# Performance work log

Measured on AMD Instinct MI355X. Metric: run time of the kernel, lower is better.

The kernel has to match this reference:

```python
import jax, jax.numpy as jnp
import numpy as np

B, C, H, W = 8, 256, 128, 128  # dim=256 channels, match_factor=2 -> num_matching=128


def setup_inputs() -> dict:
    key = jax.random.key(0)
    k1, k2 = jax.random.split(key)
    x = jax.random.normal(k1, (B, C, H, W), dtype=jnp.float32)
    Ym = jax.random.normal(k2, (B, C, H, W), dtype=jnp.float32)
    return {"x": x, "Ym": Ym, "num_matching": 128}


def _matching(x, Ym, num_matching):
    # x, Ym: (B, C, H, W); flatten spatial -> (B, C, N) with N = H*W
    b, c, h, w = x.shape
    xf = x.reshape(b, c, h * w)
    yf = Ym.reshape(b, c, h * w)
    # pairwise L2 distances between channel vectors: (B, C, C)
    x2 = jnp.sum(xf * xf, axis=-1)
    y2 = jnp.sum(yf * yf, axis=-1)
    d2 = x2[:, :, None] + y2[:, None, :] - 2.0 * jnp.einsum('bin,bjn->bij', xf, yf)
    dist = jnp.sqrt(jnp.maximum(d2, 0.0))
    # topk(k=1, largest=False) == min / argmin over candidates
    topk_values = jnp.min(dist, axis=-1)      # (B, C)
    topk_indices = jnp.argmin(dist, axis=-1)  # (B, C) nearest candidate per input channel
    # keep the num_matching input channels with smallest min-distance, in original order
    order = jnp.argsort(topk_values, axis=1)[:, :num_matching]  # channel ids with rank < num_matching
    sel = jnp.sort(order, axis=1)                               # restore original channel order (masked_select semantics)
    nn_idx = jnp.take_along_axis(topk_indices, sel, axis=1)     # (B, num_matching)
    # batched gather of candidate rows: (B, num_matching, N)
    filt = jnp.take_along_axis(yf, nn_idx[:, :, None], axis=1)
    return filt.reshape(b, num_matching, h, w)


def reference(x, Ym, num_matching):
    return _matching(x, Ym, num_matching)
```

## Files before the change

### kernel.cpp

```cpp
#include <hip/hip_runtime.h>

#define B_  8
#define C_  256
#define N_  16384
#define NM_ 128
#define LDK 40

typedef _Float16 f16x8 __attribute__((ext_vector_type(8)));
typedef float    f32x4 __attribute__((ext_vector_type(4)));

__global__ __launch_bounds__(512)
__attribute__((amdgpu_waves_per_eu(4, 4)))
void gemm_f16_kernel(const float* __restrict__ X,
                     const float* __restrict__ Y,
                     float* __restrict__ Gp,
                     float* __restrict__ x2p,
                     float* __restrict__ y2p,
                     int Kchunk) {
    __shared__ _Float16 aH[2][128][LDK];
    __shared__ _Float16 aL[2][128][LDK];
    __shared__ _Float16 bH[2][128][LDK];
    __shared__ _Float16 bL[2][128][LDK];

    int lin = blockIdx.x;
    int jt = lin & 1, it = (lin >> 1) & 1, b = (lin >> 2) & 7, ks = lin >> 5;
    int k0 = ks * Kchunk;

    int t = threadIdx.x;
    int lane = t & 63;
    int wid = t >> 6;
    int wm = wid >> 1, wn = wid & 1;

    int srow = t >> 2;
    int skq = (t & 3) * 8;

    const float* xp = X + ((size_t)(b * C_) + it * 128 + srow) * N_ + k0 + skq;
    const float* yp = Y + ((size_t)(b * C_) + jt * 128 + srow) * N_ + k0 + skq;

    f32x4 acc[2][4] = {};
    float sx = 0.f, sy = 0.f;
    float4 VA[2], VB[2];

    auto prefetch = [&](int koff) {
        VA[0] = *(const float4*)(xp + koff);
        VA[1] = *(const float4*)(xp + koff + 4);
        VB[0] = *(const float4*)(yp + koff);
        VB[1] = *(const float4*)(yp + koff + 4);
    };

    auto stage_chunk = [&](int bi) {
        _Float16 ha[8], la[8], hb[8], lb[8];
        const float* fa = (const float*)VA;
        const float* fb = (const float*)VB;
#pragma unroll
        for (int e = 0; e < 8; ++e) {
            float v = fa[e];
            _Float16 h = (_Float16)v;
            ha[e] = h; la[e] = (_Float16)(v - (float)h);
            sx += v * v;
            float w = fb[e];
            _Float16 h2 = (_Float16)w;
            hb[e] = h2; lb[e] = (_Float16)(w - (float)h2);
            sy += w * w;
        }
        *(f16x8*)&aH[bi][srow][skq] = *(f16x8*)&ha[0];
        *(f16x8*)&aL[bi][srow][skq] = *(f16x8*)&la[0];
        *(f16x8*)&bH[bi][srow][skq] = *(f16x8*)&hb[0];
        *(f16x8*)&bL[bi][srow][skq] = *(f16x8*)&lb[0];
    };

    prefetch(0);
    stage_chunk(0);
    if (Kchunk > 32) prefetch(32);

    int fr = lane & 15, fk = (lane >> 4) * 8;
    int cur = 0;

    for (int kk = 0; kk < Kchunk; kk += 32) {
        __syncthreads();

        f16x8 fAH0 = *(const f16x8*)&aH[cur][wm * 32 +  0 + fr][fk];
        f16x8 fAH1 = *(const f16x8*)&aH[cur][wm * 32 + 16 + fr][fk];
        f16x8 fAL0 = *(const f16x8*)&aL[cur][wm * 32 +  0 + fr][fk];
        f16x8 fAL1 = *(const f16x8*)&aL[cur][wm * 32 + 16 + fr][fk];

        if (kk + 32 < Kchunk) stage_chunk(cur ^ 1);
        if (kk + 64 < Kchunk) prefetch(kk + 64);

#pragma unroll
        for (int nf = 0; nf < 4; ++nf) {
            f16x8 fBH = *(const f16x8*)&bH[cur][wn * 64 + nf * 16 + fr][fk];
            f16x8 fBL = *(const f16x8*)&bL[cur][wn * 64 + nf * 16 + fr][fk];
            acc[0][nf] = __builtin_amdgcn_mfma_f32_16x16x32_f16(fAH0, fBH, acc[0][nf], 0, 0, 0);
            acc[1][nf] = __builtin_amdgcn_mfma_f32_16x16x32_f16(fAH1, fBH, acc[1][nf], 0, 0, 0);
            acc[0][nf] = __builtin_amdgcn_mfma_f32_16x16x32_f16(fAH0, fBL, acc[0][nf], 0, 0, 0);
            acc[1][nf] = __builtin_amdgcn_mfma_f32_16x16x32_f16(fAH1, fBL, acc[1][nf], 0, 0, 0);
            acc[0][nf] = __builtin_amdgcn_mfma_f32_16x16x32_f16(fAL0, fBH, acc[0][nf], 0, 0, 0);
            acc[1][nf] = __builtin_amdgcn_mfma_f32_16x16x32_f16(fAL1, fBH, acc[1][nf], 0, 0, 0);
        }
        cur ^= 1;
    }

    size_t gb = ((size_t)(ks * B_ + b) * C_ + it * 128) * C_ + jt * 128;
#pragma unroll
    for (int mf = 0; mf < 2; ++mf)
#pragma unroll
        for (int nf = 0; nf < 4; ++nf) {
            int rr = wm * 32 + mf * 16 + (lane >> 4) * 4;
            int cc = wn * 64 + nf * 16 + (lane & 15);
#pragma unroll
            for (int r = 0; r < 4; ++r)
                Gp[gb + (size_t)(rr + r) * C_ + cc] = acc[mf][nf][r];
        }

    sx += __shfl_xor(sx, 1);
    sx += __shfl_xor(sx, 2);
    sy += __shfl_xor(sy, 1);
    sy += __shfl_xor(sy, 2);
    if (!(t & 3)) {
        if (jt == 0) x2p[(ks * B_ + b) * C_ + it * 128 + srow] = sx;
        if (it == 0) y2p[(ks * B_ + b) * C_ + jt * 128 + srow] = sy;
    }
}

__global__ __launch_bounds__(256) void argmin_kernel(const float* __restrict__ Gp,
                                                     const float* __restrict__ x2p,
                                                     const float* __restrict__ y2p,
                                                     float* __restrict__ minval,
                                                     int* __restrict__ minidx,
                                                     int KS) {
    int bi = blockIdx.x;
    int b = bi >> 8;
    int i = bi & 255;
    int j = threadIdx.x;

    float g = 0.f, sx = 0.f, sy = 0.f;
    for (int ks = 0; ks < KS; ++ks) {
        g  += Gp[((size_t)(ks * B_ + b) * C_ + i) * C_ + j];
        sx += x2p[(ks * B_ + b) * C_ + i];
        sy += y2p[(ks * B_ + b) * C_ + j];
    }

    float v = sx + sy - 2.f * g;
    int idx = j;
#pragma unroll
    for (int off = 32; off > 0; off >>= 1) {
        float v2 = __shfl_down(v, off);
        int i2 = __shfl_down(idx, off);
        if (v2 < v || (v2 == v && i2 < idx)) { v = v2; idx = i2; }
    }
    __shared__ float wv[4];
    __shared__ int wi[4];
    int lane = threadIdx.x & 63, wid = threadIdx.x >> 6;
    if (lane == 0) { wv[wid] = v; wi[wid] = idx; }
    __syncthreads();
    if (threadIdx.x == 0) {
        for (int w = 1; w < 4; ++w)
            if (wv[w] < v || (wv[w] == v && wi[w] < idx)) { v = wv[w]; idx = wi[w]; }
        minval[bi] = v;
        minidx[bi] = idx;
    }
}

__global__ __launch_bounds__(256) void select_kernel(const float* __restrict__ minval,
                                                     const int* __restrict__ minidx,
                                                     int* __restrict__ nn) {
    int b = blockIdx.x;
    int i = threadIdx.x;
    __shared__ float vals[C_];
    __shared__ int wcnt[4];

    float v = minval[b * C_ + i];
    vals[i] = v;
    __syncthreads();

    int rank = 0;
    for (int tt = 0; tt < C_; ++tt) {
        float u = vals[tt];
        rank += (u < v) || (u == v && tt < i);
    }
    bool flag = rank < NM_;

    unsigned long long m = __ballot(flag);
    int lane = i & 63, wid = i >> 6;
    if (lane == 0) wcnt[wid] = (int)__popcll(m);
    __syncthreads();
    int off = 0;
    for (int w = 0; w < wid; ++w) off += wcnt[w];
    int pos = off + (int)__popcll(m & ((1ULL << lane) - 1ULL));
    if (flag) nn[b * NM_ + pos] = minidx[b * C_ + i];
}

__global__ __launch_bounds__(256) void gather_kernel(const float* __restrict__ Y,
                                                     const int* __restrict__ nn,
                                                     float* __restrict__ out) {
    int blk = blockIdx.x;
    int b = blk >> 7;
    int m = blk & 127;
    int src = nn[b * NM_ + m];
    const float4* s = (const float4*)(Y + ((size_t)b * C_ + src) * N_);
    float4* d = (float4*)(out + ((size_t)b * NM_ + m) * N_);
    for (int tt = threadIdx.x; tt < N_ / 4; tt += 256) d[tt] = s[tt];
}

extern "C" void kernel_launch(void* const* d_in, const int* in_sizes, int n_in,
                              void* d_out, int out_size, void* d_ws, size_t ws_size,
                              hipStream_t stream) {
    const float* X = (const float*)d_in[0];
    const float* Y = (const float*)d_in[1];
    float* out = (float*)d_out;

    size_t favail = ws_size / 4;
    int KS = 1;
    while (KS < 16) {
        int KS2 = KS * 2;
        size_t need = (size_t)KS2 * B_ * C_ * C_
                    + (size_t)KS2 * 2 * B_ * C_
                    + 2 * B_ * C_ + B_ * NM_;
        if (need > favail) break;
        KS = KS2;
    }
    int Kchunk = N_ / KS;

    float* minval = (float*)d_ws;
    int* minidx = (int*)(minval + B_ * C_);
    int* nn = minidx + B_ * C_;
    float* x2p = (float*)(nn + B_ * NM_);
    float* y2p = x2p + (size_t)KS * B_ * C_;
    float* Gp = y2p + (size_t)KS * B_ * C_;

    hipLaunchKernelGGL(gemm_f16_kernel, dim3(KS * 32), dim3(512), 0, stream, X, Y, Gp, x2p, y2p, Kchunk);
    hipLaunchKernelGGL(argmin_kernel, dim3(B_ * C_), dim3(256), 0, stream, Gp, x2p, y2p, minval, minidx, KS);
    hipLaunchKernelGGL(select_kernel, dim3(B_), dim3(256), 0, stream, minval, minidx, nn);
    hipLaunchKernelGGL(gather_kernel, dim3(B_ * NM_), dim3(256), 0, stream, Y, nn, out);
}
```

Measured before the change: 127.7 us.

## Widen GEMM tile to 128x256 with 16-deep K steps and XCD-aware block remap

Restructures the split-precision f16 GEMM so each block computes a 128x256 tile (all Y channels) instead of 128x128. Y is then loaded and converted once per batch/it pair rather than once per (it, jt) pair. The K step shrinks to 16 and uses the 16x16x16 MFMA. Block indices are remapped across the 8 XCDs, MFMA sections are wrapped in s_setprio, and split-K may now go up to 32 to keep enough blocks. In exchange, the larger accumulator tile raises register pressure, more K steps mean more barriers, and the bigger KS increases the partial-sum traffic the argmin kernel must read.

```diff
diff --git a/kernel.cpp b/kernel.cpp
--- a/kernel.cpp
+++ b/kernel.cpp
@@ -4,10 +4,25 @@
 #define C_  256
 #define N_  16384
 #define NM_ 128
-#define LDK 40
-
+
+typedef _Float16 f16x4 __attribute__((ext_vector_type(4)));
 typedef _Float16 f16x8 __attribute__((ext_vector_type(8)));
 typedef float    f32x4 __attribute__((ext_vector_type(4)));
+
+#define MFMA16(A, Bf, Cc) __builtin_amdgcn_mfma_f32_16x16x16f16((A), (Bf), (Cc), 0, 0, 0)
+
+#define CVT4(V, HI, LO, SQ)                                            \
+    {                                                                  \
+        float el_[4] = {(V).x, (V).y, (V).z, (V).w};                   \
+        _Pragma("unroll")                                              \
+        for (int e_ = 0; e_ < 4; ++e_) {                               \
+            float v_ = el_[e_];                                        \
+            _Float16 h_ = (_Float16)v_;                                \
+            (HI)[e_] = h_;                                             \
+            (LO)[e_] = (_Float16)(v_ - (float)h_);                     \
+            (SQ) += v_ * v_;                                           \
+        }                                                              \
+    }
 
 __global__ __launch_bounds__(512)
 __attribute__((amdgpu_waves_per_eu(4, 4)))
@@ -17,110 +32,102 @@
                      float* __restrict__ x2p,
                      float* __restrict__ y2p,
                      int Kchunk) {
-    __shared__ _Float16 aH[2][128][LDK];
-    __shared__ _Float16 aL[2][128][LDK];
-    __shared__ _Float16 bH[2][128][LDK];
-    __shared__ _Float16 bL[2][128][LDK];
-
-    int lin = blockIdx.x;
-    int jt = lin & 1, it = (lin >> 1) & 1, b = (lin >> 2) & 7, ks = lin >> 5;
+    __shared__ _Float16 aH[2][128][16];
+    __shared__ _Float16 aL[2][128][16];
+    __shared__ _Float16 bH[2][256][16];
+    __shared__ _Float16 bL[2][256][16];
+
+    int cpx = gridDim.x >> 3;
+    int lin = (blockIdx.x & 7) * cpx + (blockIdx.x >> 3);
+
+    int it = lin & 1, b = (lin >> 1) & 7, ks = lin >> 4;
     int k0 = ks * Kchunk;
+    int nsteps = Kchunk >> 4;
 
     int t = threadIdx.x;
     int lane = t & 63;
     int wid = t >> 6;
-    int wm = wid >> 1, wn = wid & 1;
-
-    int srow = t >> 2;
-    int skq = (t & 3) * 8;
-
-    const float* xp = X + ((size_t)(b * C_) + it * 128 + srow) * N_ + k0 + skq;
-    const float* yp = Y + ((size_t)(b * C_) + jt * 128 + srow) * N_ + k0 + skq;
-
-    f32x4 acc[2][4] = {};
+    int wm = wid >> 2, wn = wid & 3;
+    int fr = lane & 15, ug = lane >> 4;
+
+    int ar = t >> 2, ak = (t & 3) * 4;
+    int br = t >> 1, bk = (t & 1) * 8;
+    const float* ax = X + (size_t)(b * C_ + it * 128 + ar) * N_ + k0 + ak;
+    const float* by = Y + (size_t)(b * C_ + br) * N_ + k0 + bk;
+
+    f32x4 acc[4][4] = {};
     float sx = 0.f, sy = 0.f;
-    float4 VA[2], VB[2];
-
-    auto prefetch = [&](int koff) {
-        VA[0] = *(const float4*)(xp + koff);
-        VA[1] = *(const float4*)(xp + koff + 4);
-        VB[0] = *(const float4*)(yp + koff);
-        VB[1] = *(const float4*)(yp + koff + 4);
+    float4 vA, vB0, vB1;
+
+    auto loads = [&](int i) {
+        vA  = *(const float4*)(ax + i * 16);
+        vB0 = *(const float4*)(by + i * 16);
+        vB1 = *(const float4*)(by + i * 16 + 4);
     };
-
-    auto stage_chunk = [&](int bi) {
-        _Float16 ha[8], la[8], hb[8], lb[8];
-        const float* fa = (const float*)VA;
-        const float* fb = (const float*)VB;
-#pragma unroll
-        for (int e = 0; e < 8; ++e) {
-            float v = fa[e];
-            _Float16 h = (_Float16)v;
-            ha[e] = h; la[e] = (_Float16)(v - (float)h);
-            sx += v * v;
-            float w = fb[e];
-            _Float16 h2 = (_Float16)w;
-            hb[e] = h2; lb[e] = (_Float16)(w - (float)h2);
-            sy += w * w;
+    auto convert_store = [&](int sl) {
+        f16x4 hA, lA;
+        CVT4(vA, hA, lA, sx);
+        *(f16x4*)&aH[sl][ar][ak] = hA;
+        *(f16x4*)&aL[sl][ar][ak] = lA;
+        f16x4 h0, l0, h1, l1;
+        CVT4(vB0, h0, l0, sy);
+        CVT4(vB1, h1, l1, sy);
+        f16x8 hb, lb;
+#pragma unroll
+        for (int e = 0; e < 4; ++e) { hb[e] = h0[e]; hb[e + 4] = h1[e]; lb[e] = l0[e]; lb[e + 4] = l1[e]; }
+        *(f16x8*)&bH[sl][br][bk] = hb;
+        *(f16x8*)&bL[sl][br][bk] = lb;
+    };
+
+    loads(0);
+    convert_store(0);
+    __syncthreads();
+
+    for (int i = 0; i < nsteps; ++i) {
+        int sl = i & 1;
+        if (i + 1 < nsteps) loads(i + 1);
+
+        f16x4 aHi[4], aLo[4];
+#pragma unroll
+        for (int mf = 0; mf < 4; ++mf) {
+            aHi[mf] = *(const f16x4*)&aH[sl][wm * 64 + mf * 16 + fr][ug * 4];
+            aLo[mf] = *(const f16x4*)&aL[sl][wm * 64 + mf * 16 + fr][ug * 4];
         }
-        *(f16x8*)&aH[bi][srow][skq] = *(f16x8*)&ha[0];
-        *(f16x8*)&aL[bi][srow][skq] = *(f16x8*)&la[0];
-        *(f16x8*)&bH[bi][srow][skq] = *(f16x8*)&hb[0];
-        *(f16x8*)&bL[bi][srow][skq] = *(f16x8*)&lb[0];
-    };
-
-    prefetch(0);
-    stage_chunk(0);
-    if (Kchunk > 32) prefetch(32);
-
-    int fr = lane & 15, fk = (lane >> 4) * 8;
-    int cur = 0;
-
-    for (int kk = 0; kk < Kchunk; kk += 32) {
+        __builtin_amdgcn_s_setprio(1);
+#pragma unroll
+        for (int nf = 0; nf < 4; ++nf) {
+            f16x4 bHi = *(const f16x4*)&bH[sl][wn * 64 + nf * 16 + fr][ug * 4];
+            f16x4 bLo = *(const f16x4*)&bL[sl][wn * 64 + nf * 16 + fr][ug * 4];
+#pragma unroll
+            for (int mf = 0; mf < 4; ++mf) {
+                acc[mf][nf] = MFMA16(aHi[mf], bHi, acc[mf][nf]);
+                acc[mf][nf] = MFMA16(aHi[mf], bLo, acc[mf][nf]);
+                acc[mf][nf] = MFMA16(aLo[mf], bHi, acc[mf][nf]);
+            }
+        }
+        __builtin_amdgcn_s_setprio(0);
+
+        if (i + 1 < nsteps) convert_store(sl ^ 1);
         __syncthreads();
-
-        f16x8 fAH0 = *(const f16x8*)&aH[cur][wm * 32 +  0 + fr][fk];
-        f16x8 fAH1 = *(const f16x8*)&aH[cur][wm * 32 + 16 + fr][fk];
-        f16x8 fAL0 = *(const f16x8*)&aL[cur][wm * 32 +  0 + fr][fk];
-        f16x8 fAL1 = *(const f16x8*)&aL[cur][wm * 32 + 16 + fr][fk];
-
-        if (kk + 32 < Kchunk) stage_chunk(cur ^ 1);
-        if (kk + 64 < Kchunk) prefetch(kk + 64);
-
-#pragma unroll
-        for (int nf = 0; nf < 4; ++nf) {
-            f16x8 fBH = *(const f16x8*)&bH[cur][wn * 64 + nf * 16 + fr][fk];
-            f16x8 fBL = *(const f16x8*)&bL[cur][wn * 64 + nf * 16 + fr][fk];
-            acc[0][nf] = __builtin_amdgcn_mfma_f32_16x16x32_f16(fAH0, fBH, acc[0][nf], 0, 0, 0);
-            acc[1][nf] = __builtin_amdgcn_mfma_f32_16x16x32_f16(fAH1, fBH, acc[1][nf], 0, 0, 0);
-            acc[0][nf] = __builtin_amdgcn_mfma_f32_16x16x32_f16(fAH0, fBL, acc[0][nf], 0, 0, 0);
-            acc[1][nf] = __builtin_amdgcn_mfma_f32_16x16x32_f16(fAH1, fBL, acc[1][nf], 0, 0, 0);
-            acc[0][nf] = __builtin_amdgcn_mfma_f32_16x16x32_f16(fAL0, fBH, acc[0][nf], 0, 0, 0);
-            acc[1][nf] = __builtin_amdgcn_mfma_f32_16x16x32_f16(fAL1, fBH, acc[1][nf], 0, 0, 0);
-        }
-        cur ^= 1;
-    }
-
-    size_t gb = ((size_t)(ks * B_ + b) * C_ + it * 128) * C_ + jt * 128;
-#pragma unroll
-    for (int mf = 0; mf < 2; ++mf)
-#pragma unroll
-        for (int nf = 0; nf < 4; ++nf) {
-            int rr = wm * 32 + mf * 16 + (lane >> 4) * 4;
-            int cc = wn * 64 + nf * 16 + (lane & 15);
-#pragma unroll
-            for (int r = 0; r < 4; ++r)
-                Gp[gb + (size_t)(rr + r) * C_ + cc] = acc[mf][nf][r];
-        }
+    }
 
     sx += __shfl_xor(sx, 1);
     sx += __shfl_xor(sx, 2);
+    if ((t & 3) == 0) x2p[(ks * B_ + b) * C_ + it * 128 + ar] = sx;
     sy += __shfl_xor(sy, 1);
-    sy += __shfl_xor(sy, 2);
-    if (!(t & 3)) {
-        if (jt == 0) x2p[(ks * B_ + b) * C_ + it * 128 + srow] = sx;
-        if (it == 0) y2p[(ks * B_ + b) * C_ + jt * 128 + srow] = sy;
-    }
+    if (it == 0 && (t & 1) == 0) y2p[(ks * B_ + b) * C_ + br] = sy;
+
+    size_t gbase = ((size_t)(ks * B_ + b) * C_ + it * 128) * C_;
+#pragma unroll
+    for (int mf = 0; mf < 4; ++mf)
+#pragma unroll
+        for (int nf = 0; nf < 4; ++nf) {
+            int rr = wm * 64 + mf * 16 + (lane >> 4) * 4;
+            int cc = wn * 64 + nf * 16 + (lane & 15);
+#pragma unroll
+            for (int r = 0; r < 4; ++r)
+                Gp[gbase + (size_t)(rr + r) * C_ + cc] = acc[mf][nf][r];
+        }
 }
 
 __global__ __launch_bounds__(256) void argmin_kernel(const float* __restrict__ Gp,
@@ -212,7 +219,7 @@
 
     size_t favail = ws_size / 4;
     int KS = 1;
-    while (KS < 16) {
+    while (KS < 32) {
         int KS2 = KS * 2;
         size_t need = (size_t)KS2 * B_ * C_ * C_
                     + (size_t)KS2 * 2 * B_ * C_
@@ -229,7 +236,7 @@
     float* y2p = x2p + (size_t)KS * B_ * C_;
     float* Gp = y2p + (size_t)KS * B_ * C_;
 
-    hipLaunchKernelGGL(gemm_f16_kernel, dim3(KS * 32), dim3(512), 0, stream, X, Y, Gp, x2p, y2p, Kchunk);
+    hipLaunchKernelGGL(gemm_f16_kernel, dim3(KS * 16), dim3(512), 0, stream, X, Y, Gp, x2p, y2p, Kchunk);
     hipLaunchKernelGGL(argmin_kernel, dim3(B_ * C_), dim3(256), 0, stream, Gp, x2p, y2p, minval, minidx, KS);
     hipLaunchKernelGGL(select_kernel, dim3(B_), dim3(256), 0, stream, minval, minidx, nn);
     hipLaunchKernelGGL(gather_kernel, dim3(B_ * NM_), dim3(256), 0, stream, Y, nn, out);
```

New measurement: 164.7 us. 29.0% more time.
